# Performance work log

Measured on AMD Instinct MI355X. Metric: run time of the kernel, lower is better.

Reference implementation:

```python
import jax, jax.numpy as jnp
import numpy as np

N_NODES = 100000
N_EDGES = 3200000
N_GRAPHS = 256
HID = 32
IN_DIM = 6
BN_EPS = 1e-5


def setup_inputs() -> dict:
    key = jax.random.key(0)
    ks = jax.random.split(key, 24)
    inp = {}
    inp['x'] = jax.random.normal(ks[0], (N_NODES, IN_DIM), dtype=jnp.float32)
    inp['edge_index'] = jax.random.randint(ks[1], (2, N_EDGES), 0, N_NODES)
    inp['pos'] = jax.random.normal(ks[2], (N_NODES, 6), dtype=jnp.float32)
    inp['batch'] = jnp.sort(jax.random.randint(ks[3], (N_NODES,), 0, N_GRAPHS))
    # GaussKernel params
    inp['inv_sigma1'] = jax.random.uniform(ks[4], (1,)) * 0.02 + 0.99
    inp['inv_sigma2'] = jax.random.uniform(ks[5], (1,)) * 0.02 + 0.99
    # GCNConv weights (glorot-ish scale) + biases
    dims = [IN_DIM, HID, HID, HID, HID]
    for i in range(4):
        s = 1.0 / np.sqrt(dims[i])
        inp[f'W{i+1}'] = jax.random.normal(ks[6 + i], (dims[i], dims[i + 1]), dtype=jnp.float32) * s
        inp[f'b{i+1}'] = jnp.zeros((dims[i + 1],), dtype=jnp.float32)
    # BatchNorm (layers 1..3 only; last layer has no BN) - eval mode params
    for i in range(3):
        inp[f'g{i+1}'] = jnp.ones((HID,), dtype=jnp.float32)
        inp[f'be{i+1}'] = jnp.zeros((HID,), dtype=jnp.float32)
    # post-MP linear HID -> 1
    inp['Wout'] = jax.random.normal(ks[20], (HID, 1), dtype=jnp.float32) * (1.0 / np.sqrt(HID))
    inp['bout'] = jnp.zeros((1,), dtype=jnp.float32)
    return inp


def _gauss_kernel(pos, row, col, s1, s2):
    p1, p2 = pos[row, :3], pos[col, :3]
    a1, a2 = pos[row, 3:], pos[col, 3:]
    D = jnp.sum((p1 - p2) ** 2, axis=-1)               # [E]
    T = (1.0 - jnp.sum(a1 * a2, axis=-1)) ** 2         # [E]
    return jnp.exp(-(D * s1[0] ** 2 + T * s2[0] ** 2))  # [E]


def _gcn_conv(x, W, b, row, col, ew):
    # PyG GCNConv (normalize=True, add_self_loops=True, fill_value=1.0)
    n = x.shape[0]
    xw = x @ W                                          # [N, out]
    deg = jnp.zeros((n,), xw.dtype).at[col].add(ew) + 1.0  # self-loop weight 1
    dinv = jnp.where(deg > 0, deg ** -0.5, 0.0)
    norm = dinv[row] * ew * dinv[col]                   # [E]
    out = jnp.zeros_like(xw).at[col].add(norm[:, None] * xw[row])
    out = out + (dinv * dinv)[:, None] * xw             # self-loop messages
    return out + b


def _bn_eval(x, g, be):
    # running_mean=0, running_var=1 at init (inference mode)
    return x * (g / jnp.sqrt(1.0 + BN_EPS)) + be


def reference(x, edge_index, pos, batch, inv_sigma1, inv_sigma2,
              W1, b1, W2, b2, W3, b3, W4, b4,
              g1, be1, g2, be2, g3, be3, Wout, bout):
    row, col = edge_index[0], edge_index[1]
    ew = _gauss_kernel(pos, row, col, inv_sigma1, inv_sigma2)
    # layer 1..3: GCN -> BN -> ReLU (dropout is identity in eval)
    h = x
    for (W, b, g, be) in ((W1, b1, g1, be1), (W2, b2, g2, be2), (W3, b3, g3, be3)):
        h = _gcn_conv(h, W, b, row, col, ew)
        h = jax.nn.relu(_bn_eval(h, g, be))
    # layer 4: plain GCN (no BN / act / dropout)
    h = _gcn_conv(h, W4, b4, row, col, ew)
    emb = h
    # graph task: global mean pool then Linear + Sigmoid
    sums = jax.ops.segment_sum(h, batch, num_segments=N_GRAPHS)
    cnts = jax.ops.segment_sum(jnp.ones((h.shape[0],), h.dtype), batch, num_segments=N_GRAPHS)
    pooled = sums / jnp.maximum(cnts, 1.0)[:, None]
    pred = jax.nn.sigmoid(pooled @ Wout + bout)
    return (emb, pred)
```

## Files before the change

kernel.cpp:

```cpp
#include <hip/hip_runtime.h>
#include <hip/hip_bf16.h>
#include <math.h>

#define TB 256
#define PCHUNK 1024
#define SLOTS 80

__device__ __forceinline__ void atomic_add_f32(float* p, float v) {
    unsafeAtomicAdd(p, v);
}

__device__ __forceinline__ unsigned short f2bf(float x) {
    unsigned u = __float_as_uint(x);
    return (unsigned short)((u + 0x7FFF + ((u >> 16) & 1)) >> 16);
}
__device__ __forceinline__ float4 bf4(ushort4 u) {
    return make_float4(__uint_as_float((unsigned)u.x << 16),
                       __uint_as_float((unsigned)u.y << 16),
                       __uint_as_float((unsigned)u.z << 16),
                       __uint_as_float((unsigned)u.w << 16));
}

__global__ __launch_bounds__(TB) void zero_pack_kernel(int* __restrict__ hist,
                                                       float* __restrict__ sums,
                                                       float* __restrict__ cnt,
                                                       const float2* __restrict__ pos2,
                                                       float4* __restrict__ pos8,
                                                       int n_nodes) {
    int i = blockIdx.x * TB + threadIdx.x;
    if (i < n_nodes) {
        hist[i] = 0;
        float2 a = pos2[i * 3 + 0], b = pos2[i * 3 + 1], c = pos2[i * 3 + 2];
        pos8[i * 2 + 0] = make_float4(a.x, a.y, b.x, b.y);
        pos8[i * 2 + 1] = make_float4(c.x, c.y, 0.f, 0.f);
    }
    if (i < 256 * 32) sums[i] = 0.0f;
    if (i < 256) cnt[i] = 0.0f;
}

__global__ __launch_bounds__(TB) void edge_weight_kernel(
    const int* __restrict__ row, const int* __restrict__ col,
    const float4* __restrict__ pos8,
    const float* __restrict__ s1p, const float* __restrict__ s2p,
    int* __restrict__ hist, int2* __restrict__ csr, int n_edges) {
    int e = blockIdx.x * TB + threadIdx.x;
    if (e >= n_edges) return;
    int r = row[e], c = col[e];
    float4 ra = pos8[r * 2 + 0], rb = pos8[r * 2 + 1];
    float4 ca = pos8[c * 2 + 0], cb = pos8[c * 2 + 1];
    float dx = ra.x - ca.x, dy = ra.y - ca.y, dz = ra.z - ca.z;
    float D = dx * dx + dy * dy + dz * dz;
    float dot = ra.w * ca.w + rb.x * cb.x + rb.y * cb.y;
    float t = 1.0f - dot;
    float s1 = s1p[0], s2 = s2p[0];
    float w = expf(-(D * s1 * s1 + t * t * s2 * s2));
    int rank = atomicAdd(&hist[c], 1);
    if (rank < SLOTS)
        csr[(size_t)c * SLOTS + rank] = make_int2(r, __float_as_int(w));
}

__global__ __launch_bounds__(TB) void segfill_kernel(
    const int* __restrict__ hist, int2* __restrict__ csr, int n_nodes) {
    int c = blockIdx.x * TB + threadIdx.x;
    if (c >= n_nodes) return;
    int cnt = min(hist[c], SLOTS);
    int nseg = (cnt + 7) >> 3;
    size_t base = (size_t)c * SLOTS;
    for (int j = cnt; j < nseg * 8; j++) csr[base + j] = make_int2(0, 0);
}

__global__ __launch_bounds__(TB) void deg_dinv_kernel(
    const int* __restrict__ hist, const int2* __restrict__ csr,
    float* __restrict__ dinv, int n_nodes) {
    int t = blockIdx.x * TB + threadIdx.x;
    int c = t >> 3, f = t & 7;
    if (c >= n_nodes) return;
    int cnt = min(hist[c], SLOTS);
    size_t base = (size_t)c * SLOTS;
    float s = 0.0f;
    for (int i = f; i < cnt; i += 8) s += __int_as_float(csr[base + i].y);
    s += __shfl_down(s, 4, 8);
    s += __shfl_down(s, 2, 8);
    s += __shfl_down(s, 1, 8);
    if (f == 0) dinv[c] = rsqrtf(s + 1.0f);
}

template <int K, bool BN>
__global__ __launch_bounds__(TB) void matmul_kernel(
    const float* __restrict__ fin, const float* __restrict__ W,
    const float* __restrict__ g, const float* __restrict__ be,
    const float* __restrict__ dinv, unsigned short* __restrict__ ywb,
    int n_nodes) {
    __shared__ float Ws[K * 32];
    __shared__ float gs[32];
    __shared__ float bs[32];
    int tid = threadIdx.x;
    for (int i = tid; i < K * 32; i += TB) Ws[i] = W[i];
    if (BN && tid < 32) {
        gs[tid] = g[tid] * (1.0f / sqrtf(1.0f + 1e-5f));
        bs[tid] = be[tid];
    }
    __syncthreads();
    int n = blockIdx.x * TB + tid;
    if (n >= n_nodes) return;
    float vals[K];
    const float* fp = fin + (size_t)n * K;
    if (K % 4 == 0) {
#pragma unroll
        for (int k = 0; k < K / 4; k++) {
            float4 v = ((const float4*)fp)[k];
            vals[k * 4 + 0] = v.x;
            vals[k * 4 + 1] = v.y;
            vals[k * 4 + 2] = v.z;
            vals[k * 4 + 3] = v.w;
        }
    } else {
#pragma unroll
        for (int k = 0; k < K; k++) vals[k] = fp[k];
    }
    if (BN) {
#pragma unroll
        for (int k = 0; k < K; k++) vals[k] = fmaxf(fmaf(vals[k], gs[k], bs[k]), 0.0f);
    }
    float acc[32];
#pragma unroll
    for (int j = 0; j < 32; j++) acc[j] = 0.0f;
#pragma unroll
    for (int k = 0; k < K; k++) {
        float v = vals[k];
#pragma unroll
        for (int j = 0; j < 32; j++) acc[j] = fmaf(v, Ws[k * 32 + j], acc[j]);
    }
    float di = dinv[n];
    uint4* op = (uint4*)(ywb + (size_t)n * 32);
#pragma unroll
    for (int j = 0; j < 4; j++) {
        uint4 pk;
        pk.x = (unsigned)f2bf(di * acc[j * 8 + 0]) | ((unsigned)f2bf(di * acc[j * 8 + 1]) << 16);
        pk.y = (unsigned)f2bf(di * acc[j * 8 + 2]) | ((unsigned)f2bf(di * acc[j * 8 + 3]) << 16);
        pk.z = (unsigned)f2bf(di * acc[j * 8 + 4]) | ((unsigned)f2bf(di * acc[j * 8 + 5]) << 16);
        pk.w = (unsigned)f2bf(di * acc[j * 8 + 6]) | ((unsigned)f2bf(di * acc[j * 8 + 7]) << 16);
        op[j] = pk;
    }
}

__device__ __forceinline__ float4 f4_fma(float w, float4 v, float4 a) {
    return make_float4(fmaf(w, v.x, a.x), fmaf(w, v.y, a.y),
                       fmaf(w, v.z, a.z), fmaf(w, v.w, a.w));
}

__global__ __launch_bounds__(TB) void gather_node_kernel(
    const int* __restrict__ hist, const int2* __restrict__ csr,
    const unsigned short* __restrict__ ywb, const float* __restrict__ dinv,
    const float4* __restrict__ bias4, float* __restrict__ agg, int n_nodes) {
    int n = blockIdx.x * (TB / 32) + (threadIdx.x >> 5);
    if (n >= n_nodes) return;
    int lane = threadIdx.x & 31;
    int o = lane >> 3, f4i = (lane & 7) * 4;
    int nseg = (min(hist[n], SLOTS) + 7) >> 3;
    size_t base = (size_t)n * SLOTS;
    float4 acc = make_float4(0.f, 0.f, 0.f, 0.f);
    for (int seg = o; seg < nseg; seg += 4) {
        const int4* q = (const int4*)(csr + base + (size_t)seg * 8);
        int4 q0 = q[0], q1 = q[1], q2 = q[2], q3 = q[3];
        ushort4 u0 = *(const ushort4*)(ywb + ((size_t)q0.x << 5) + f4i);
        ushort4 u1 = *(const ushort4*)(ywb + ((size_t)q0.z << 5) + f4i);
        ushort4 u2 = *(const ushort4*)(ywb + ((size_t)q1.x << 5) + f4i);
        ushort4 u3 = *(const ushort4*)(ywb + ((size_t)q1.z << 5) + f4i);
        ushort4 u4 = *(const ushort4*)(ywb + ((size_t)q2.x << 5) + f4i);
        ushort4 u5 = *(const ushort4*)(ywb + ((size_t)q2.z << 5) + f4i);
        ushort4 u6 = *(const ushort4*)(ywb + ((size_t)q3.x << 5) + f4i);
        ushort4 u7 = *(const ushort4*)(ywb + ((size_t)q3.z << 5) + f4i);
        acc = f4_fma(__int_as_float(q0.y), bf4(u0), acc);
        acc = f4_fma(__int_as_float(q0.w), bf4(u1), acc);
        acc = f4_fma(__int_as_float(q1.y), bf4(u2), acc);
        acc = f4_fma(__int_as_float(q1.w), bf4(u3), acc);
        acc = f4_fma(__int_as_float(q2.y), bf4(u4), acc);
        acc = f4_fma(__int_as_float(q2.w), bf4(u5), acc);
        acc = f4_fma(__int_as_float(q3.y), bf4(u6), acc);
        acc = f4_fma(__int_as_float(q3.w), bf4(u7), acc);
    }
    {
        float4 t;
        t.x = __shfl_xor(acc.x, 8, 32); t.y = __shfl_xor(acc.y, 8, 32);
        t.z = __shfl_xor(acc.z, 8, 32); t.w = __shfl_xor(acc.w, 8, 32);
        acc.x += t.x; acc.y += t.y; acc.z += t.z; acc.w += t.w;
        t.x = __shfl_xor(acc.x, 16, 32); t.y = __shfl_xor(acc.y, 16, 32);
        t.z = __shfl_xor(acc.z, 16, 32); t.w = __shfl_xor(acc.w, 16, 32);
        acc.x += t.x; acc.y += t.y; acc.z += t.z; acc.w += t.w;
    }
    if (o == 0) {
        float di = dinv[n];
        ushort4 us = *(const ushort4*)(ywb + ((size_t)n << 5) + f4i);
        float4 self = bf4(us);
        float4 bb = bias4[f4i >> 2];
        float4 v;
        v.x = fmaf(di, acc.x + self.x, bb.x);
        v.y = fmaf(di, acc.y + self.y, bb.y);
        v.z = fmaf(di, acc.z + self.z, bb.z);
        v.w = fmaf(di, acc.w + self.w, bb.w);
        ((float4*)agg)[(size_t)n * 8 + (f4i >> 2)] = v;
    }
}

__global__ __launch_bounds__(TB) void pool_kernel(
    const float* __restrict__ agg, const int* __restrict__ batch,
    float* __restrict__ sums, float* __restrict__ cnt, int n_nodes) {
    int j = threadIdx.x & 31;
    int s = threadIdx.x >> 5;
    int base = blockIdx.x * PCHUNK;
    int endn = min(base + PCHUNK, n_nodes);
    float acc = 0.0f;
    float cacc = 0.0f;
    int cur = -1;
    for (int n = base + s; n < endn; n += 8) {
        int bg = batch[n];
        float v = agg[(size_t)n * 32 + j];
        if (bg != cur) {
            if (cur >= 0) {
                atomic_add_f32(&sums[(size_t)cur * 32 + j], acc);
                if (j == 0) atomic_add_f32(&cnt[cur], cacc);
            }
            cur = bg; acc = 0.0f; cacc = 0.0f;
        }
        acc += v;
        cacc += 1.0f;
    }
    if (cur >= 0) {
        atomic_add_f32(&sums[(size_t)cur * 32 + j], acc);
        if (j == 0) atomic_add_f32(&cnt[cur], cacc);
    }
}

__global__ __launch_bounds__(TB) void pred_kernel(
    const float* __restrict__ sums, const float* __restrict__ cnt,
    const float* __restrict__ Wout, const float* __restrict__ bout,
    float* __restrict__ out) {
    int g = blockIdx.x * TB + threadIdx.x;
    if (g >= 256) return;
    float c = fmaxf(cnt[g], 1.0f);
    float acc = 0.0f;
#pragma unroll
    for (int j = 0; j < 32; j++) acc += sums[g * 32 + j] * Wout[j];
    float z = acc / c + bout[0];
    out[g] = 1.0f / (1.0f + expf(-z));
}

extern "C" void kernel_launch(void* const* d_in, const int* in_sizes, int n_in,
                              void* d_out, int out_size, void* d_ws, size_t ws_size,
                              hipStream_t stream) {
    const float* x = (const float*)d_in[0];
    const int* edge_index = (const int*)d_in[1];
    const float* pos = (const float*)d_in[2];
    const int* batch = (const int*)d_in[3];
    const float* s1 = (const float*)d_in[4];
    const float* s2 = (const float*)d_in[5];
    const float* W1 = (const float*)d_in[6];
    const float* b1 = (const float*)d_in[7];
    const float* W2 = (const float*)d_in[8];
    const float* b2 = (const float*)d_in[9];
    const float* W3 = (const float*)d_in[10];
    const float* b3 = (const float*)d_in[11];
    const float* W4 = (const float*)d_in[12];
    const float* b4 = (const float*)d_in[13];
    const float* g1 = (const float*)d_in[14];
    const float* be1 = (const float*)d_in[15];
    const float* g2 = (const float*)d_in[16];
    const float* be2 = (const float*)d_in[17];
    const float* g3 = (const float*)d_in[18];
    const float* be3 = (const float*)d_in[19];
    const float* Wout = (const float*)d_in[20];
    const float* bout = (const float*)d_in[21];

    const size_t E = (size_t)in_sizes[1] / 2;
    const size_t N = (size_t)in_sizes[3];

    const int* row = edge_index;
    const int* col = edge_index + E;

    auto align256 = [](size_t v) { return (v + 255) & ~(size_t)255; };
    char* w = (char*)d_ws;
    int2* csr = (int2*)w;      w += align256(N * SLOTS * 8);
    int* hist = (int*)w;       w += align256(N * 4);
    unsigned short* ywb = (unsigned short*)w; w += align256(N * 32 * 2);
    float* aggB = (float*)w;   w += align256(N * 32 * 4);
    float4* pos8 = (float4*)w; w += align256(N * 8 * 4);
    float* dinv = (float*)w;   w += align256(N * 4);
    float* sums = (float*)w;   w += align256(256 * 32 * 4);
    float* cnt = (float*)w;    w += align256(256 * 4);

    float* out_emb = (float*)d_out;
    float* out_pred = (float*)d_out + N * 32;

    const int gN = (int)((N + TB - 1) / TB);
    const int gE = (int)((E + TB - 1) / TB);
    const int gN8 = (int)((N * 8 + TB - 1) / TB);
    const int gW = (int)((N + (TB / 32) - 1) / (TB / 32));
    const int gP = (int)((N + PCHUNK - 1) / PCHUNK);

    zero_pack_kernel<<<gN, TB, 0, stream>>>(hist, sums, cnt, (const float2*)pos,
                                            pos8, (int)N);
    edge_weight_kernel<<<gE, TB, 0, stream>>>(row, col, pos8, s1, s2,
                                              hist, csr, (int)E);
    segfill_kernel<<<gN, TB, 0, stream>>>(hist, csr, (int)N);
    deg_dinv_kernel<<<gN8, TB, 0, stream>>>(hist, csr, dinv, (int)N);

    matmul_kernel<6, false><<<gN, TB, 0, stream>>>(x, W1, nullptr, nullptr, dinv,
                                                   ywb, (int)N);
    gather_node_kernel<<<gW, TB, 0, stream>>>(hist, csr, ywb, dinv,
                                              (const float4*)b1, aggB, (int)N);
    matmul_kernel<32, true><<<gN, TB, 0, stream>>>(aggB, W2, g1, be1, dinv, ywb, (int)N);
    gather_node_kernel<<<gW, TB, 0, stream>>>(hist, csr, ywb, dinv,
                                              (const float4*)b2, aggB, (int)N);
    matmul_kernel<32, true><<<gN, TB, 0, stream>>>(aggB, W3, g2, be2, dinv, ywb, (int)N);
    gather_node_kernel<<<gW, TB, 0, stream>>>(hist, csr, ywb, dinv,
                                              (const float4*)b3, aggB, (int)N);
    matmul_kernel<32, true><<<gN, TB, 0, stream>>>(aggB, W4, g3, be3, dinv, ywb, (int)N);
    gather_node_kernel<<<gW, TB, 0, stream>>>(hist, csr, ywb, dinv,
                                              (const float4*)b4, out_emb, (int)N);

    pool_kernel<<<gP, TB, 0, stream>>>(out_emb, batch, sums, cnt, (int)N);
    pred_kernel<<<1, TB, 0, stream>>>(sums, cnt, Wout, bout, out_pred);
}
```

Measured before the change: 538.2 us.

## Fuse BN+ReLU+next-layer matmul into gather kernel and use nontemporal CSR stores

The gather kernel for layers 1-3 now applies BN and ReLU and multiplies by the next layer's weights in place, using lane shuffles within each 32-lane group. It writes the bf16 dinv-scaled features straight to a ping-pong buffer, so the fp32 intermediate round trip and three matmul launches go away. CSR entries in the edge kernel are now written as packed 64-bit nontemporal stores. In exchange the gather kernels carry extra shuffle and FMA work and shared-memory weight loads per block, and the nontemporal stores may hurt the reuse of CSR lines in cache.

After: 566.1 us. +5.2%, slower.

```diff
diff --git a/kernel.cpp b/kernel.cpp
--- a/kernel.cpp
+++ b/kernel.cpp
@@ -55,8 +55,12 @@
     float s1 = s1p[0], s2 = s2p[0];
     float w = expf(-(D * s1 * s1 + t * t * s2 * s2));
     int rank = atomicAdd(&hist[c], 1);
-    if (rank < SLOTS)
-        csr[(size_t)c * SLOTS + rank] = make_int2(r, __float_as_int(w));
+    if (rank < SLOTS) {
+        unsigned long long pk =
+            ((unsigned long long)__float_as_uint(w) << 32) | (unsigned)r;
+        __builtin_nontemporal_store(
+            pk, (unsigned long long*)(csr + (size_t)c * SLOTS + rank));
+    }
 }
 
 __global__ __launch_bounds__(TB) void segfill_kernel(
@@ -85,43 +89,21 @@
     if (f == 0) dinv[c] = rsqrtf(s + 1.0f);
 }
 
-template <int K, bool BN>
+template <int K>
 __global__ __launch_bounds__(TB) void matmul_kernel(
     const float* __restrict__ fin, const float* __restrict__ W,
-    const float* __restrict__ g, const float* __restrict__ be,
     const float* __restrict__ dinv, unsigned short* __restrict__ ywb,
     int n_nodes) {
     __shared__ float Ws[K * 32];
-    __shared__ float gs[32];
-    __shared__ float bs[32];
     int tid = threadIdx.x;
     for (int i = tid; i < K * 32; i += TB) Ws[i] = W[i];
-    if (BN && tid < 32) {
-        gs[tid] = g[tid] * (1.0f / sqrtf(1.0f + 1e-5f));
-        bs[tid] = be[tid];
-    }
     __syncthreads();
     int n = blockIdx.x * TB + tid;
     if (n >= n_nodes) return;
     float vals[K];
     const float* fp = fin + (size_t)n * K;
-    if (K % 4 == 0) {
-#pragma unroll
-        for (int k = 0; k < K / 4; k++) {
-            float4 v = ((const float4*)fp)[k];
-            vals[k * 4 + 0] = v.x;
-            vals[k * 4 + 1] = v.y;
-            vals[k * 4 + 2] = v.z;
-            vals[k * 4 + 3] = v.w;
-        }
-    } else {
-#pragma unroll
-        for (int k = 0; k < K; k++) vals[k] = fp[k];
-    }
-    if (BN) {
-#pragma unroll
-        for (int k = 0; k < K; k++) vals[k] = fmaxf(fmaf(vals[k], gs[k], bs[k]), 0.0f);
-    }
+#pragma unroll
+    for (int k = 0; k < K; k++) vals[k] = fp[k];
     float acc[32];
 #pragma unroll
     for (int j = 0; j < 32; j++) acc[j] = 0.0f;
@@ -149,14 +131,9 @@
                        fmaf(w, v.z, a.z), fmaf(w, v.w, a.w));
 }
 
-__global__ __launch_bounds__(TB) void gather_node_kernel(
-    const int* __restrict__ hist, const int2* __restrict__ csr,
-    const unsigned short* __restrict__ ywb, const float* __restrict__ dinv,
-    const float4* __restrict__ bias4, float* __restrict__ agg, int n_nodes) {
-    int n = blockIdx.x * (TB / 32) + (threadIdx.x >> 5);
-    if (n >= n_nodes) return;
-    int lane = threadIdx.x & 31;
-    int o = lane >> 3, f4i = (lane & 7) * 4;
+__device__ __forceinline__ float4 gather_core(
+    const int* hist, const int2* csr, const unsigned short* ywb,
+    const float* dinv, const float4* bias4, int n, int o, int f4i) {
     int nseg = (min(hist[n], SLOTS) + 7) >> 3;
     size_t base = (size_t)n * SLOTS;
     float4 acc = make_float4(0.f, 0.f, 0.f, 0.f);
@@ -180,27 +157,84 @@
         acc = f4_fma(__int_as_float(q3.y), bf4(u6), acc);
         acc = f4_fma(__int_as_float(q3.w), bf4(u7), acc);
     }
-    {
-        float4 t;
-        t.x = __shfl_xor(acc.x, 8, 32); t.y = __shfl_xor(acc.y, 8, 32);
-        t.z = __shfl_xor(acc.z, 8, 32); t.w = __shfl_xor(acc.w, 8, 32);
-        acc.x += t.x; acc.y += t.y; acc.z += t.z; acc.w += t.w;
-        t.x = __shfl_xor(acc.x, 16, 32); t.y = __shfl_xor(acc.y, 16, 32);
-        t.z = __shfl_xor(acc.z, 16, 32); t.w = __shfl_xor(acc.w, 16, 32);
-        acc.x += t.x; acc.y += t.y; acc.z += t.z; acc.w += t.w;
+    float4 t;
+    t.x = __shfl_xor(acc.x, 8, 32); t.y = __shfl_xor(acc.y, 8, 32);
+    t.z = __shfl_xor(acc.z, 8, 32); t.w = __shfl_xor(acc.w, 8, 32);
+    acc.x += t.x; acc.y += t.y; acc.z += t.z; acc.w += t.w;
+    t.x = __shfl_xor(acc.x, 16, 32); t.y = __shfl_xor(acc.y, 16, 32);
+    t.z = __shfl_xor(acc.z, 16, 32); t.w = __shfl_xor(acc.w, 16, 32);
+    acc.x += t.x; acc.y += t.y; acc.z += t.z; acc.w += t.w;
+    float di = dinv[n];
+    ushort4 us = *(const ushort4*)(ywb + ((size_t)n << 5) + f4i);
+    float4 self = bf4(us);
+    float4 bb = bias4[f4i >> 2];
+    float4 v;
+    v.x = fmaf(di, acc.x + self.x, bb.x);
+    v.y = fmaf(di, acc.y + self.y, bb.y);
+    v.z = fmaf(di, acc.z + self.z, bb.z);
+    v.w = fmaf(di, acc.w + self.w, bb.w);
+    return v;
+}
+
+__global__ __launch_bounds__(TB) void gather_fused_kernel(
+    const int* __restrict__ hist, const int2* __restrict__ csr,
+    const unsigned short* __restrict__ ywb_in, const float* __restrict__ dinv,
+    const float4* __restrict__ bias4, const float* __restrict__ W,
+    const float* __restrict__ g, const float* __restrict__ be,
+    unsigned short* __restrict__ ywb_out, int n_nodes) {
+    __shared__ float Ws[32 * 32];
+    __shared__ float gs[32];
+    __shared__ float bs[32];
+    int tid = threadIdx.x;
+    for (int i = tid; i < 32 * 32; i += TB) Ws[i] = W[i];
+    if (tid < 32) {
+        gs[tid] = g[tid] * (1.0f / sqrtf(1.0f + 1e-5f));
+        bs[tid] = be[tid];
+    }
+    __syncthreads();
+    int n = blockIdx.x * (TB / 32) + (tid >> 5);
+    if (n >= n_nodes) return;
+    int lane = tid & 31;
+    int o = lane >> 3, f4i = (lane & 7) * 4;
+    float4 v = gather_core(hist, csr, ywb_in, dinv, bias4, n, o, f4i);
+    float4 vb;
+    vb.x = fmaxf(fmaf(v.x, gs[f4i + 0], bs[f4i + 0]), 0.0f);
+    vb.y = fmaxf(fmaf(v.y, gs[f4i + 1], bs[f4i + 1]), 0.0f);
+    vb.z = fmaxf(fmaf(v.z, gs[f4i + 2], bs[f4i + 2]), 0.0f);
+    vb.w = fmaxf(fmaf(v.w, gs[f4i + 3], bs[f4i + 3]), 0.0f);
+    float4 out = make_float4(0.f, 0.f, 0.f, 0.f);
+#pragma unroll
+    for (int gg = 0; gg < 8; gg++) {
+        float4 vg;
+        vg.x = __shfl(vb.x, gg, 32);
+        vg.y = __shfl(vb.y, gg, 32);
+        vg.z = __shfl(vb.z, gg, 32);
+        vg.w = __shfl(vb.w, gg, 32);
+        out = f4_fma(vg.x, *(const float4*)(Ws + (4 * gg + 0) * 32 + f4i), out);
+        out = f4_fma(vg.y, *(const float4*)(Ws + (4 * gg + 1) * 32 + f4i), out);
+        out = f4_fma(vg.z, *(const float4*)(Ws + (4 * gg + 2) * 32 + f4i), out);
+        out = f4_fma(vg.w, *(const float4*)(Ws + (4 * gg + 3) * 32 + f4i), out);
     }
     if (o == 0) {
         float di = dinv[n];
-        ushort4 us = *(const ushort4*)(ywb + ((size_t)n << 5) + f4i);
-        float4 self = bf4(us);
-        float4 bb = bias4[f4i >> 2];
-        float4 v;
-        v.x = fmaf(di, acc.x + self.x, bb.x);
-        v.y = fmaf(di, acc.y + self.y, bb.y);
-        v.z = fmaf(di, acc.z + self.z, bb.z);
-        v.w = fmaf(di, acc.w + self.w, bb.w);
-        ((float4*)agg)[(size_t)n * 8 + (f4i >> 2)] = v;
-    }
+        uint2 pk;
+        pk.x = (unsigned)f2bf(di * out.x) | ((unsigned)f2bf(di * out.y) << 16);
+        pk.y = (unsigned)f2bf(di * out.z) | ((unsigned)f2bf(di * out.w) << 16);
+        *(uint2*)(ywb_out + ((size_t)n << 5) + f4i) = pk;
+    }
+}
+
+__global__ __launch_bounds__(TB) void gather_final_kernel(
+    const int* __restrict__ hist, const int2* __restrict__ csr,
+    const unsigned short* __restrict__ ywb_in, const float* __restrict__ dinv,
+    const float4* __restrict__ bias4, float* __restrict__ agg, int n_nodes) {
+    int tid = threadIdx.x;
+    int n = blockIdx.x * (TB / 32) + (tid >> 5);
+    if (n >= n_nodes) return;
+    int lane = tid & 31;
+    int o = lane >> 3, f4i = (lane & 7) * 4;
+    float4 v = gather_core(hist, csr, ywb_in, dinv, bias4, n, o, f4i);
+    if (o == 0) ((float4*)agg)[(size_t)n * 8 + (f4i >> 2)] = v;
 }
 
 __global__ __launch_bounds__(TB) void pool_kernel(
@@ -282,8 +316,8 @@
     char* w = (char*)d_ws;
     int2* csr = (int2*)w;      w += align256(N * SLOTS * 8);
     int* hist = (int*)w;       w += align256(N * 4);
-    unsigned short* ywb = (unsigned short*)w; w += align256(N * 32 * 2);
-    float* aggB = (float*)w;   w += align256(N * 32 * 4);
+    unsigned short* ywbA = (unsigned short*)w; w += align256(N * 32 * 2);
+    unsigned short* ywbB = (unsigned short*)w; w += align256(N * 32 * 2);
     float4* pos8 = (float4*)w; w += align256(N * 8 * 4);
     float* dinv = (float*)w;   w += align256(N * 4);
     float* sums = (float*)w;   w += align256(256 * 32 * 4);
@@ -305,19 +339,18 @@
     segfill_kernel<<<gN, TB, 0, stream>>>(hist, csr, (int)N);
     deg_dinv_kernel<<<gN8, TB, 0, stream>>>(hist, csr, dinv, (int)N);
 
-    matmul_kernel<6, false><<<gN, TB, 0, stream>>>(x, W1, nullptr, nullptr, dinv,
-                                                   ywb, (int)N);
-    gather_node_kernel<<<gW, TB, 0, stream>>>(hist, csr, ywb, dinv,
-                                              (const float4*)b1, aggB, (int)N);
-    matmul_kernel<32, true><<<gN, TB, 0, stream>>>(aggB, W2, g1, be1, dinv, ywb, (int)N);
-    gather_node_kernel<<<gW, TB, 0, stream>>>(hist, csr, ywb, dinv,
-                                              (const float4*)b2, aggB, (int)N);
-    matmul_kernel<32, true><<<gN, TB, 0, stream>>>(aggB, W3, g2, be2, dinv, ywb, (int)N);
-    gather_node_kernel<<<gW, TB, 0, stream>>>(hist, csr, ywb, dinv,
-                                              (const float4*)b3, aggB, (int)N);
-    matmul_kernel<32, true><<<gN, TB, 0, stream>>>(aggB, W4, g3, be3, dinv, ywb, (int)N);
-    gather_node_kernel<<<gW, TB, 0, stream>>>(hist, csr, ywb, dinv,
-                                              (const float4*)b4, out_emb, (int)N);
+    matmul_kernel<6><<<gN, TB, 0, stream>>>(x, W1, dinv, ywbA, (int)N);
+    gather_fused_kernel<<<gW, TB, 0, stream>>>(hist, csr, ywbA, dinv,
+                                               (const float4*)b1, W2, g1, be1,
+                                               ywbB, (int)N);
+    gather_fused_kernel<<<gW, TB, 0, stream>>>(hist, csr, ywbB, dinv,
+                                               (const float4*)b2, W3, g2, be2,
+                                               ywbA, (int)N);
+    gather_fused_kernel<<<gW, TB, 0, stream>>>(hist, csr, ywbA, dinv,
+                                               (const float4*)b3, W4, g3, be3,
+                                               ywbB, (int)N);
+    gather_final_kernel<<<gW, TB, 0, stream>>>(hist, csr, ywbB, dinv,
+                                               (const float4*)b4, out_emb, (int)N);
 
     pool_kernel<<<gP, TB, 0, stream>>>(out_emb, batch, sums, cnt, (int)N);
     pred_kernel<<<1, TB, 0, stream>>>(sums, cnt, Wout, bout, out_pred);
```
